# Optimization experiments

Hardware: AMD Instinct MI355X
Metric: run time of the kernel (lower is better)

## Reference

```python
import jax, jax.numpy as jnp
import numpy as np

B, S, D, H = 4, 2048, 1024, 16
DH = D // H  # 64

def setup_inputs() -> dict:
    key = jax.random.key(0)
    k0, k1, k2, k3 = jax.random.split(key, 4)
    x = jax.random.normal(k0, (B, S, D), dtype=jnp.float32)
    # Linear layers use random_normal init, shape (D, D), no bias.
    Wq = jax.random.normal(k1, (D, D), dtype=jnp.float32) * 0.05
    Wk = jax.random.normal(k2, (D, D), dtype=jnp.float32) * 0.05
    Wv = jax.random.normal(k3, (D, D), dtype=jnp.float32) * 0.05
    return {"encoder_input": x, "Wq": Wq, "Wk": Wk, "Wv": Wv}

def reference(encoder_input, Wq, Wk, Wv):
    x = encoder_input
    n_heads = H
    # Per-document projections, batched: [B,S,D]
    q = jnp.einsum('bsd,de->bse', x, Wq)
    k = jnp.einsum('bsd,de->bse', x, Wk)
    v = jnp.einsum('bsd,de->bse', x, Wv)
    # np.split(..., H, axis=-1) == reshape last dim to [H, DH]
    q = q.reshape(B, S, n_heads, DH)
    k = k.reshape(B, S, n_heads, DH)
    v = v.reshape(B, S, n_heads, DH)
    # Scaled dot-product attention; NOTE: original divides by N_HEADS, not sqrt(d_head)
    scores = jnp.einsum('bqhd,bkhd->bhqk', q, k) / jnp.float32(n_heads)
    attn = jax.nn.softmax(scores, axis=-1)
    out = jnp.einsum('bhqk,bkhd->bqhd', attn, v)
    # Concatenate heads along last dim -> [B,S,D]
    return out.reshape(B, S, D)
```

## Files before the change

### kernel.cpp

```cpp
#include <hip/hip_runtime.h>

typedef unsigned short u16;
typedef unsigned int   u32;
typedef __bf16 bf16x8 __attribute__((ext_vector_type(8)));
typedef __bf16 bf16x4 __attribute__((ext_vector_type(4)));
typedef float  f32x4  __attribute__((ext_vector_type(4)));
typedef u32    u32x4  __attribute__((ext_vector_type(4)));
typedef u32    u32x2  __attribute__((ext_vector_type(2)));
typedef u16    u16x8  __attribute__((ext_vector_type(8)));

#define MFMA16(a,b,c) __builtin_amdgcn_mfma_f32_16x16x32_bf16(a,b,c,0,0,0)

#define BB 4
#define SS 2048
#define DD 1024
#define HH 16
#define DH 64
#define MM 8192

#define QSCALE 0.0901684400555602f

#define WAIT_VM0() __builtin_amdgcn_s_waitcnt(0x0F70)

__device__ __forceinline__ u16 f2bf(float f) {
  u32 u = __builtin_bit_cast(u32, f);
  u += 0x7fffu + ((u >> 16) & 1u);
  return (u16)(u >> 16);
}

__device__ __forceinline__ void async16(const void* g, void* l) {
  __builtin_amdgcn_global_load_lds(
      (const __attribute__((address_space(1))) unsigned int*)g,
      (__attribute__((address_space(3))) unsigned int*)l, 16, 0, 0);
}

__global__ __launch_bounds__(256) void convert_x(
    const float* __restrict__ in, u16* __restrict__ out)
{
  const size_t stride = (size_t)gridDim.x * 256 * 8;
  for (size_t i = ((size_t)blockIdx.x * 256 + threadIdx.x) * 8;
       i < (size_t)MM * DD; i += stride) {
    f32x4 a = *(const f32x4*)(in + i);
    f32x4 b = *(const f32x4*)(in + i + 4);
    u32x2 ua = __builtin_bit_cast(u32x2, __builtin_convertvector(a, bf16x4));
    u32x2 ub = __builtin_bit_cast(u32x2, __builtin_convertvector(b, bf16x4));
    u32x4 v = {ua[0], ua[1], ub[0], ub[1]};
    *(u32x4*)(out + i) = v;
  }
}

__global__ __launch_bounds__(256) void fill_sig(float* __restrict__ out, int n)
{
  for (int i = blockIdx.x * 256 + threadIdx.x; i < n; i += gridDim.x * 256)
    out[i] = 3.0f;
}

__global__ __launch_bounds__(256) void convert_w(
    const float* __restrict__ w0, const float* __restrict__ w1,
    const float* __restrict__ w2, u16* __restrict__ WtAll)
{
  const int z = blockIdx.z;
  const float* W = (z == 0) ? w0 : ((z == 1) ? w1 : w2);
  u16* Wt = WtAll + (size_t)z * DD * DD;
  const int n0 = blockIdx.x * 64;
  const int k0 = blockIdx.y * 64;
  __shared__ u16 tile[64][65];
#pragma unroll
  for (int i = 0; i < 16; ++i) {
    int e = threadIdx.x + i * 256;
    int r = e >> 6, c = e & 63;
    tile[r][c] = f2bf(W[(size_t)(k0 + r) * DD + n0 + c]);
  }
  __syncthreads();
#pragma unroll
  for (int i = 0; i < 16; ++i) {
    int e = threadIdx.x + i * 256;
    int r = e >> 6, c = e & 63;
    Wt[(size_t)(n0 + r) * DD + k0 + c] = tile[c][r];
  }
}

__global__ __launch_bounds__(256) void qkv_gemm(
    const u16* __restrict__ X, const u16* __restrict__ WtAll,
    u16* __restrict__ QKV)
{
  const int z = blockIdx.z;
  const u16* Wt = WtAll + (size_t)z * DD * DD;
  u16* Y = QKV + (size_t)z * MM * DD;
  const int m0 = blockIdx.x * 128;
  const int n0 = blockIdx.y * 128;
  const int t = threadIdx.x;
  const int ln = t & 63;
  const int w  = t >> 6;
  const int cl = ln & 15;
  const int qd = ln >> 4;
  const int wm = (w & 1) * 64;
  const int wn = (w >> 1) * 64;
  const int srow   = ln >> 2;
  const int schunk = (ln & 3) * 8;

  __shared__ __align__(16) u16 Asm[128 * 32];
  __shared__ __align__(16) u16 Bsm[128 * 32];

  const f32x4 fzero = {0.f, 0.f, 0.f, 0.f};
  f32x4 acc[4][4];
#pragma unroll
  for (int i = 0; i < 4; ++i)
#pragma unroll
    for (int j = 0; j < 4; ++j) acc[i][j] = fzero;

  for (int k0 = 0; k0 < DD; k0 += 32) {
    __syncthreads();
#pragma unroll
    for (int c = 0; c < 2; ++c) {
      async16(X  + (size_t)(m0 + c * 64 + w * 16 + srow) * DD + k0 + schunk,
              Asm + (c * 64 + w * 16) * 32);
      async16(Wt + (size_t)(n0 + c * 64 + w * 16 + srow) * DD + k0 + schunk,
              Bsm + (c * 64 + w * 16) * 32);
    }
    WAIT_VM0();
    __syncthreads();

    bf16x8 af[4], bf[4];
#pragma unroll
    for (int mb = 0; mb < 4; ++mb)
      af[mb] = *(const bf16x8*)&Asm[(wm + mb * 16 + cl) * 32 + qd * 8];
#pragma unroll
    for (int nb = 0; nb < 4; ++nb)
      bf[nb] = *(const bf16x8*)&Bsm[(wn + nb * 16 + cl) * 32 + qd * 8];
#pragma unroll
    for (int mb = 0; mb < 4; ++mb)
#pragma unroll
      for (int nb = 0; nb < 4; ++nb)
        acc[mb][nb] = MFMA16(af[mb], bf[nb], acc[mb][nb]);
  }

  const float scl = (z == 0) ? QSCALE : 1.0f;
#pragma unroll
  for (int mb = 0; mb < 4; ++mb) {
#pragma unroll
    for (int r = 0; r < 4; ++r) {
      const size_t row = (size_t)(m0 + wm + mb * 16 + qd * 4 + r) * DD;
      f32x4 v = {acc[mb][0][r] * scl, acc[mb][1][r] * scl,
                 acc[mb][2][r] * scl, acc[mb][3][r] * scl};
      bf16x4 bv = __builtin_convertvector(v, bf16x4);
#pragma unroll
      for (int nb = 0; nb < 4; ++nb)
        *(__bf16*)&Y[row + n0 + wn + nb * 16 + cl] = bv[nb];
    }
  }
}

__global__ __launch_bounds__(256) void vtrans(
    const u16* __restrict__ V, u16* __restrict__ VtG)
{
  const int b = blockIdx.z;
  const int h = blockIdx.y;
  const int s0 = blockIdx.x * 64;
  __shared__ u16 tile[64][65];
#pragma unroll
  for (int i = 0; i < 16; ++i) {
    int e = threadIdx.x + i * 256;
    int r = e >> 6, c = e & 63;
    tile[r][c] = V[(size_t)(b * SS + s0 + r) * DD + h * DH + c];
  }
  __syncthreads();
#pragma unroll
  for (int i = 0; i < 16; ++i) {
    int e = threadIdx.x + i * 256;
    int r = e >> 6, c = e & 63;
    VtG[((size_t)(b * HH + h) * DH + r) * SS + s0 + c] = tile[c][r];
  }
}

__global__ __launch_bounds__(256, 2) void attn_kernel(
    const u16* __restrict__ QKV, const u16* __restrict__ VtG,
    float* __restrict__ Out)
{
  const int bh = blockIdx.x;
  const int b = bh >> 4;
  const int h = bh & 15;
  const int q0 = blockIdx.y * 128;
  const int t = threadIdx.x;
  const int ln = t & 63;
  const int w  = t >> 6;
  const int cl = ln & 15;
  const int qd = ln >> 4;
  const int srow   = ln >> 2;
  const int schunk = (ln & 3) * 8;

  const u16* Qg = QKV;
  const u16* Kg = QKV + (size_t)MM * DD;

  __shared__ __align__(16) u16 smem[20992];
  u16* const Pl = smem + 16384;

  const size_t qoffA = (size_t)(b * SS + q0 + w * 16 + cl) * DD + h * DH;
  const size_t qoffB = qoffA + (size_t)64 * DD;
  const bf16x8 qfA0 = *(const bf16x8*)(Qg + qoffA + qd * 8);
  const bf16x8 qfA1 = *(const bf16x8*)(Qg + qoffA + 32 + qd * 8);
  const bf16x8 qfB0 = *(const bf16x8*)(Qg + qoffB + qd * 8);
  const bf16x8 qfB1 = *(const bf16x8*)(Qg + qoffB + 32 + qd * 8);

  const f32x4 fzero = {0.f, 0.f, 0.f, 0.f};
  f32x4 oaccA[4], oaccB[4];
#pragma unroll
  for (int mt = 0; mt < 4; ++mt) { oaccA[mt] = fzero; oaccB[mt] = fzero; }
  float lsumA = 0.f, lsumB = 0.f;

  const size_t kgbase  = (size_t)b * SS * DD + (size_t)h * DH;
  const size_t vtgbase = ((size_t)(b * HH + h)) * DH * SS;

  u16* const Pw  = Pl + (w * 16 + cl) * 72;
  const u16* const Pr = Pl + (w * 16 + cl) * 72;

  auto stage = [&](int kt, int bi) {
    u16* kb = smem + bi * 4096;
    u16* vb = smem + 8192 + bi * 4096;
#pragma unroll
    for (int s = 0; s < 2; ++s) {
      async16(Kg  + kgbase + (size_t)(kt + w * 16 + srow) * DD + s * 32 + schunk,
              kb + (s * 64 + w * 16) * 32);
      async16(VtG + vtgbase + (size_t)(w * 16 + srow) * SS + kt + s * 32 + schunk,
              vb + (s * 64 + w * 16) * 32);
    }
  };

  stage(0, 0);

  for (int it = 0; it < SS / 64; ++it) {
    const int cur = it & 1;
    WAIT_VM0();
    __syncthreads();
    if (it + 1 < SS / 64) stage((it + 1) * 64, cur ^ 1);

    const u16* Kh = smem + cur * 4096;
    const u16* Vh = smem + 8192 + cur * 4096;

    f32x4 stA[4], stB[4];
#pragma unroll
    for (int mt = 0; mt < 4; ++mt) {
      bf16x8 kf0 = *(const bf16x8*)&Kh[(mt * 16 + cl) * 32 + qd * 8];
      bf16x8 kf1 = *(const bf16x8*)&Kh[(64 + mt * 16 + cl) * 32 + qd * 8];
      f32x4 za = fzero, zb = fzero;
      za = MFMA16(kf0, qfA0, za); za = MFMA16(kf1, qfA1, za);
      zb = MFMA16(kf0, qfB0, zb); zb = MFMA16(kf1, qfB1, zb);
      stA[mt] = za; stB[mt] = zb;
    }

    bf16x8 vf0[4], vf1[4];
#pragma unroll
    for (int mt = 0; mt < 4; ++mt) {
      vf0[mt] = *(const bf16x8*)&Vh[(mt * 16 + cl) * 32 + qd * 8];
      vf1[mt] = *(const bf16x8*)&Vh[(64 + mt * 16 + cl) * 32 + qd * 8];
    }

#pragma unroll
    for (int mt = 0; mt < 4; ++mt) {
      f32x4 p;
#pragma unroll
      for (int r = 0; r < 4; ++r) {
        p[r] = __builtin_amdgcn_exp2f(stA[mt][r]);
        lsumA += p[r];
      }
      *(u32x2*)(Pw + mt * 16 + qd * 4) =
          __builtin_bit_cast(u32x2, __builtin_convertvector(p, bf16x4));
    }

    f32x4 pB[4];
#pragma unroll
    for (int mt = 0; mt < 4; ++mt) {
#pragma unroll
      for (int r = 0; r < 4; ++r) {
        pB[mt][r] = __builtin_amdgcn_exp2f(stB[mt][r]);
        lsumB += pB[mt][r];
      }
    }

    {
      const bf16x8 pf0 = *(const bf16x8*)(Pr + qd * 8);
      const bf16x8 pf1 = *(const bf16x8*)(Pr + 32 + qd * 8);
#pragma unroll
      for (int mt = 0; mt < 4; ++mt) {
        oaccA[mt] = MFMA16(vf0[mt], pf0, oaccA[mt]);
        oaccA[mt] = MFMA16(vf1[mt], pf1, oaccA[mt]);
      }
    }

#pragma unroll
    for (int mt = 0; mt < 4; ++mt)
      *(u32x2*)(Pw + mt * 16 + qd * 4) =
          __builtin_bit_cast(u32x2, __builtin_convertvector(pB[mt], bf16x4));
    {
      const bf16x8 pf0 = *(const bf16x8*)(Pr + qd * 8);
      const bf16x8 pf1 = *(const bf16x8*)(Pr + 32 + qd * 8);
#pragma unroll
      for (int mt = 0; mt < 4; ++mt) {
        oaccB[mt] = MFMA16(vf0[mt], pf0, oaccB[mt]);
        oaccB[mt] = MFMA16(vf1[mt], pf1, oaccB[mt]);
      }
    }
  }

  lsumA += __shfl_xor(lsumA, 16);
  lsumA += __shfl_xor(lsumA, 32);
  lsumB += __shfl_xor(lsumB, 16);
  lsumB += __shfl_xor(lsumB, 32);

  __syncthreads();
  float* Ol = (float*)smem;
  const int q   = ln >> 2;
  const int seg = ln & 3;
  const float* src = Ol + w * 1088 + q * 68 + seg * 16;

  const float invA = 1.f / lsumA;
#pragma unroll
  for (int mt = 0; mt < 4; ++mt) {
    f32x4 vv = oaccA[mt];
#pragma unroll
    for (int r = 0; r < 4; ++r) vv[r] *= invA;
    *(f32x4*)(Ol + w * 1088 + cl * 68 + mt * 16 + qd * 4) = vv;
  }
  {
    float* dst = Out + (size_t)(b * SS + q0 + w * 16 + q) * DD + h * DH + seg * 16;
#pragma unroll
    for (int i = 0; i < 4; ++i)
      *(f32x4*)(dst + i * 4) = *(const f32x4*)(src + i * 4);
  }

  const float invB = 1.f / lsumB;
#pragma unroll
  for (int mt = 0; mt < 4; ++mt) {
    f32x4 vv = oaccB[mt];
#pragma unroll
    for (int r = 0; r < 4; ++r) vv[r] *= invB;
    *(f32x4*)(Ol + w * 1088 + cl * 68 + mt * 16 + qd * 4) = vv;
  }
  {
    float* dst = Out + (size_t)(b * SS + q0 + 64 + w * 16 + q) * DD + h * DH + seg * 16;
#pragma unroll
    for (int i = 0; i < 4; ++i)
      *(f32x4*)(dst + i * 4) = *(const f32x4*)(src + i * 4);
  }
}

extern "C" void kernel_launch(void* const* d_in, const int* in_sizes, int n_in,
                              void* d_out, int out_size, void* d_ws, size_t ws_size,
                              hipStream_t stream)
{
  const float* x  = (const float*)d_in[0];
  const float* wq = (const float*)d_in[1];
  const float* wk = (const float*)d_in[2];
  const float* wv = (const float*)d_in[3];
  float* out = (float*)d_out;

  const size_t need = ((size_t)MM * DD + 3 * (size_t)DD * DD +
                       3 * (size_t)MM * DD + (size_t)MM * DD) * sizeof(u16);
  if (ws_size < need) {
    fill_sig<<<1024, 256, 0, stream>>>(out, out_size);
    return;
  }

  u16* xs  = (u16*)d_ws;
  u16* wt  = xs + (size_t)MM * DD;
  u16* qkv = wt + (size_t)3 * DD * DD;
  u16* vtg = qkv + (size_t)3 * MM * DD;

  convert_x<<<2048, 256, 0, stream>>>(x, xs);
  convert_w<<<dim3(16, 16, 3), 256, 0, stream>>>(wq, wk, wv, wt);
  qkv_gemm<<<dim3(64, 8, 3), 256, 0, stream>>>(xs, wt, qkv);
  vtrans<<<dim3(32, HH, BB), 256, 0, stream>>>(qkv + (size_t)2 * MM * DD, vtg);
  attn_kernel<<<dim3(HH * BB, SS / 128, 1), 256, 0, stream>>>(qkv, vtg, out);
}
```

Measured before the change: 243.7 us.

## Widen GEMM K-tile, double attention query tile, swizzle K/V shared memory

The QKV GEMM now stages 64-wide K slices per barrier instead of 32, which halves the number of sync/wait rounds. The attention kernel processes 256 queries per block instead of 128, so each staged K/V tile is reused across four query groups and global K/V traffic drops. K and V tiles are also XOR-swizzled in shared memory to reduce LDS bank conflicts. In exchange, register pressure goes up (four output accumulators), which may lower occupancy, and the grid has fewer blocks.

```diff
diff --git a/kernel.cpp b/kernel.cpp
--- a/kernel.cpp
+++ b/kernel.cpp
@@ -96,11 +96,11 @@
   const int qd = ln >> 4;
   const int wm = (w & 1) * 64;
   const int wn = (w >> 1) * 64;
-  const int srow   = ln >> 2;
-  const int schunk = (ln & 3) * 8;
-
-  __shared__ __align__(16) u16 Asm[128 * 32];
-  __shared__ __align__(16) u16 Bsm[128 * 32];
+  const int srow8   = ln >> 3;
+  const int schunk8 = (ln & 7) * 8;
+
+  __shared__ __align__(16) u16 Asm[128 * 64];
+  __shared__ __align__(16) u16 Bsm[128 * 64];
 
   const f32x4 fzero = {0.f, 0.f, 0.f, 0.f};
   f32x4 acc[4][4];
@@ -109,30 +109,33 @@
 #pragma unroll
     for (int j = 0; j < 4; ++j) acc[i][j] = fzero;
 
-  for (int k0 = 0; k0 < DD; k0 += 32) {
+  for (int k0 = 0; k0 < DD; k0 += 64) {
     __syncthreads();
 #pragma unroll
-    for (int c = 0; c < 2; ++c) {
-      async16(X  + (size_t)(m0 + c * 64 + w * 16 + srow) * DD + k0 + schunk,
-              Asm + (c * 64 + w * 16) * 32);
-      async16(Wt + (size_t)(n0 + c * 64 + w * 16 + srow) * DD + k0 + schunk,
-              Bsm + (c * 64 + w * 16) * 32);
+    for (int c = 0; c < 4; ++c) {
+      async16(X  + (size_t)(m0 + c * 32 + w * 8 + srow8) * DD + k0 + schunk8,
+              Asm + (c * 32 + w * 8) * 64);
+      async16(Wt + (size_t)(n0 + c * 32 + w * 8 + srow8) * DD + k0 + schunk8,
+              Bsm + (c * 32 + w * 8) * 64);
     }
     WAIT_VM0();
     __syncthreads();
 
-    bf16x8 af[4], bf[4];
-#pragma unroll
-    for (int mb = 0; mb < 4; ++mb)
-      af[mb] = *(const bf16x8*)&Asm[(wm + mb * 16 + cl) * 32 + qd * 8];
-#pragma unroll
-    for (int nb = 0; nb < 4; ++nb)
-      bf[nb] = *(const bf16x8*)&Bsm[(wn + nb * 16 + cl) * 32 + qd * 8];
-#pragma unroll
-    for (int mb = 0; mb < 4; ++mb)
+#pragma unroll
+    for (int kk = 0; kk < 2; ++kk) {
+      bf16x8 af[4], bf[4];
+#pragma unroll
+      for (int mb = 0; mb < 4; ++mb)
+        af[mb] = *(const bf16x8*)&Asm[(wm + mb * 16 + cl) * 64 + kk * 32 + qd * 8];
 #pragma unroll
       for (int nb = 0; nb < 4; ++nb)
-        acc[mb][nb] = MFMA16(af[mb], bf[nb], acc[mb][nb]);
+        bf[nb] = *(const bf16x8*)&Bsm[(wn + nb * 16 + cl) * 64 + kk * 32 + qd * 8];
+#pragma unroll
+      for (int mb = 0; mb < 4; ++mb)
+#pragma unroll
+        for (int nb = 0; nb < 4; ++nb)
+          acc[mb][nb] = MFMA16(af[mb], bf[nb], acc[mb][nb]);
+    }
   }
 
   const float scl = (z == 0) ? QSCALE : 1.0f;
@@ -180,14 +183,15 @@
   const int bh = blockIdx.x;
   const int b = bh >> 4;
   const int h = bh & 15;
-  const int q0 = blockIdx.y * 128;
+  const int q0 = blockIdx.y * 256;
   const int t = threadIdx.x;
   const int ln = t & 63;
   const int w  = t >> 6;
   const int cl = ln & 15;
   const int qd = ln >> 4;
-  const int srow   = ln >> 2;
-  const int schunk = (ln & 3) * 8;
+  const int srow = ln >> 2;
+  const int swz = (((ln & 3) ^ ((srow >> 1) & 3)) << 3);
+  const int sx = ((qd ^ ((cl >> 1) & 3)) << 3);
 
   const u16* Qg = QKV;
   const u16* Kg = QKV + (size_t)MM * DD;
@@ -195,18 +199,23 @@
   __shared__ __align__(16) u16 smem[20992];
   u16* const Pl = smem + 16384;
 
-  const size_t qoffA = (size_t)(b * SS + q0 + w * 16 + cl) * DD + h * DH;
-  const size_t qoffB = qoffA + (size_t)64 * DD;
-  const bf16x8 qfA0 = *(const bf16x8*)(Qg + qoffA + qd * 8);
-  const bf16x8 qfA1 = *(const bf16x8*)(Qg + qoffA + 32 + qd * 8);
-  const bf16x8 qfB0 = *(const bf16x8*)(Qg + qoffB + qd * 8);
-  const bf16x8 qfB1 = *(const bf16x8*)(Qg + qoffB + 32 + qd * 8);
+  const size_t qoff0 = (size_t)(b * SS + q0 + w * 16 + cl) * DD + h * DH;
+  const bf16x8 qf0a = *(const bf16x8*)(Qg + qoff0 + qd * 8);
+  const bf16x8 qf0b = *(const bf16x8*)(Qg + qoff0 + 32 + qd * 8);
+  const bf16x8 qf1a = *(const bf16x8*)(Qg + qoff0 + (size_t)64 * DD + qd * 8);
+  const bf16x8 qf1b = *(const bf16x8*)(Qg + qoff0 + (size_t)64 * DD + 32 + qd * 8);
+  const bf16x8 qf2a = *(const bf16x8*)(Qg + qoff0 + (size_t)128 * DD + qd * 8);
+  const bf16x8 qf2b = *(const bf16x8*)(Qg + qoff0 + (size_t)128 * DD + 32 + qd * 8);
+  const bf16x8 qf3a = *(const bf16x8*)(Qg + qoff0 + (size_t)192 * DD + qd * 8);
+  const bf16x8 qf3b = *(const bf16x8*)(Qg + qoff0 + (size_t)192 * DD + 32 + qd * 8);
 
   const f32x4 fzero = {0.f, 0.f, 0.f, 0.f};
-  f32x4 oaccA[4], oaccB[4];
-#pragma unroll
-  for (int mt = 0; mt < 4; ++mt) { oaccA[mt] = fzero; oaccB[mt] = fzero; }
-  float lsumA = 0.f, lsumB = 0.f;
+  f32x4 oacc0[4], oacc1[4], oacc2[4], oacc3[4];
+#pragma unroll
+  for (int mt = 0; mt < 4; ++mt) {
+    oacc0[mt] = fzero; oacc1[mt] = fzero; oacc2[mt] = fzero; oacc3[mt] = fzero;
+  }
+  float lsum0 = 0.f, lsum1 = 0.f, lsum2 = 0.f, lsum3 = 0.f;
 
   const size_t kgbase  = (size_t)b * SS * DD + (size_t)h * DH;
   const size_t vtgbase = ((size_t)(b * HH + h)) * DH * SS;
@@ -219,12 +228,67 @@
     u16* vb = smem + 8192 + bi * 4096;
 #pragma unroll
     for (int s = 0; s < 2; ++s) {
-      async16(Kg  + kgbase + (size_t)(kt + w * 16 + srow) * DD + s * 32 + schunk,
+      async16(Kg  + kgbase + (size_t)(kt + w * 16 + srow) * DD + s * 32 + swz,
               kb + (s * 64 + w * 16) * 32);
-      async16(VtG + vtgbase + (size_t)(w * 16 + srow) * SS + kt + s * 32 + schunk,
+      async16(VtG + vtgbase + (size_t)(w * 16 + srow) * SS + kt + s * 32 + swz,
               vb + (s * 64 + w * 16) * 32);
     }
   };
+
+#define PAIR(QA0, QA1, QB0, QB1, OA, OB, LA, LB) do {                         \
+    f32x4 stA[4], stB[4];                                                     \
+    _Pragma("unroll")                                                         \
+    for (int mt = 0; mt < 4; ++mt) {                                          \
+      bf16x8 kf0 = *(const bf16x8*)&Kh[(mt * 16 + cl) * 32 + sx];             \
+      bf16x8 kf1 = *(const bf16x8*)&Kh[(64 + mt * 16 + cl) * 32 + sx];        \
+      f32x4 za = fzero, zb = fzero;                                           \
+      za = MFMA16(kf0, QA0, za); za = MFMA16(kf1, QA1, za);                   \
+      zb = MFMA16(kf0, QB0, zb); zb = MFMA16(kf1, QB1, zb);                   \
+      stA[mt] = za; stB[mt] = zb;                                             \
+    }                                                                         \
+    _Pragma("unroll")                                                         \
+    for (int mt = 0; mt < 4; ++mt) {                                          \
+      f32x4 p;                                                                \
+      _Pragma("unroll")                                                       \
+      for (int r = 0; r < 4; ++r) {                                           \
+        p[r] = __builtin_amdgcn_exp2f(stA[mt][r]);                            \
+        LA += p[r];                                                           \
+      }                                                                       \
+      *(u32x2*)(Pw + mt * 16 + qd * 4) =                                      \
+          __builtin_bit_cast(u32x2, __builtin_convertvector(p, bf16x4));      \
+    }                                                                         \
+    f32x4 pB[4];                                                              \
+    _Pragma("unroll")                                                         \
+    for (int mt = 0; mt < 4; ++mt) {                                          \
+      _Pragma("unroll")                                                       \
+      for (int r = 0; r < 4; ++r) {                                           \
+        pB[mt][r] = __builtin_amdgcn_exp2f(stB[mt][r]);                       \
+        LB += pB[mt][r];                                                      \
+      }                                                                       \
+    }                                                                         \
+    {                                                                         \
+      const bf16x8 pf0 = *(const bf16x8*)(Pr + qd * 8);                       \
+      const bf16x8 pf1 = *(const bf16x8*)(Pr + 32 + qd * 8);                  \
+      _Pragma("unroll")                                                       \
+      for (int mt = 0; mt < 4; ++mt) {                                        \
+        OA[mt] = MFMA16(vf0[mt], pf0, OA[mt]);                                \
+        OA[mt] = MFMA16(vf1[mt], pf1, OA[mt]);                                \
+      }                                                                       \
+    }                                                                         \
+    _Pragma("unroll")                                                         \
+    for (int mt = 0; mt < 4; ++mt)                                            \
+      *(u32x2*)(Pw + mt * 16 + qd * 4) =                                      \
+          __builtin_bit_cast(u32x2, __builtin_convertvector(pB[mt], bf16x4)); \
+    {                                                                         \
+      const bf16x8 pf0 = *(const bf16x8*)(Pr + qd * 8);                       \
+      const bf16x8 pf1 = *(const bf16x8*)(Pr + 32 + qd * 8);                  \
+      _Pragma("unroll")                                                       \
+      for (int mt = 0; mt < 4; ++mt) {                                        \
+        OB[mt] = MFMA16(vf0[mt], pf0, OB[mt]);                                \
+        OB[mt] = MFMA16(vf1[mt], pf1, OB[mt]);                                \
+      }                                                                       \
+    }                                                                         \
+  } while (0)
 
   stage(0, 0);
 
@@ -237,75 +301,21 @@
     const u16* Kh = smem + cur * 4096;
     const u16* Vh = smem + 8192 + cur * 4096;
 
-    f32x4 stA[4], stB[4];
+    bf16x8 vf0[4], vf1[4];
 #pragma unroll
     for (int mt = 0; mt < 4; ++mt) {
-      bf16x8 kf0 = *(const bf16x8*)&Kh[(mt * 16 + cl) * 32 + qd * 8];
-      bf16x8 kf1 = *(const bf16x8*)&Kh[(64 + mt * 16 + cl) * 32 + qd * 8];
-      f32x4 za = fzero, zb = fzero;
-      za = MFMA16(kf0, qfA0, za); za = MFMA16(kf1, qfA1, za);
-      zb = MFMA16(kf0, qfB0, zb); zb = MFMA16(kf1, qfB1, zb);
-      stA[mt] = za; stB[mt] = zb;
-    }
-
-    bf16x8 vf0[4], vf1[4];
-#pragma unroll
-    for (int mt = 0; mt < 4; ++mt) {
-      vf0[mt] = *(const bf16x8*)&Vh[(mt * 16 + cl) * 32 + qd * 8];
-      vf1[mt] = *(const bf16x8*)&Vh[(64 + mt * 16 + cl) * 32 + qd * 8];
-    }
-
-#pragma unroll
-    for (int mt = 0; mt < 4; ++mt) {
-      f32x4 p;
-#pragma unroll
-      for (int r = 0; r < 4; ++r) {
-        p[r] = __builtin_amdgcn_exp2f(stA[mt][r]);
-        lsumA += p[r];
-      }
-      *(u32x2*)(Pw + mt * 16 + qd * 4) =
-          __builtin_bit_cast(u32x2, __builtin_convertvector(p, bf16x4));
-    }
-
-    f32x4 pB[4];
-#pragma unroll
-    for (int mt = 0; mt < 4; ++mt) {
-#pragma unroll
-      for (int r = 0; r < 4; ++r) {
-        pB[mt][r] = __builtin_amdgcn_exp2f(stB[mt][r]);
-        lsumB += pB[mt][r];
-      }
-    }
-
-    {
-      const bf16x8 pf0 = *(const bf16x8*)(Pr + qd * 8);
-      const bf16x8 pf1 = *(const bf16x8*)(Pr + 32 + qd * 8);
-#pragma unroll
-      for (int mt = 0; mt < 4; ++mt) {
-        oaccA[mt] = MFMA16(vf0[mt], pf0, oaccA[mt]);
-        oaccA[mt] = MFMA16(vf1[mt], pf1, oaccA[mt]);
-      }
-    }
-
-#pragma unroll
-    for (int mt = 0; mt < 4; ++mt)
-      *(u32x2*)(Pw + mt * 16 + qd * 4) =
-          __builtin_bit_cast(u32x2, __builtin_convertvector(pB[mt], bf16x4));
-    {
-      const bf16x8 pf0 = *(const bf16x8*)(Pr + qd * 8);
-      const bf16x8 pf1 = *(const bf16x8*)(Pr + 32 + qd * 8);
-#pragma unroll
-      for (int mt = 0; mt < 4; ++mt) {
-        oaccB[mt] = MFMA16(vf0[mt], pf0, oaccB[mt]);
-        oaccB[mt] = MFMA16(vf1[mt], pf1, oaccB[mt]);
-      }
-    }
-  }
-
-  lsumA += __shfl_xor(lsumA, 16);
-  lsumA += __shfl_xor(lsumA, 32);
-  lsumB += __shfl_xor(lsumB, 16);
-  lsumB += __shfl_xor(lsumB, 32);
+      vf0[mt] = *(const bf16x8*)&Vh[(mt * 16 + cl) * 32 + sx];
+      vf1[mt] = *(const bf16x8*)&Vh[(64 + mt * 16 + cl) * 32 + sx];
+    }
+
+    PAIR(qf0a, qf0b, qf1a, qf1b, oacc0, oacc1, lsum0, lsum1);
+    PAIR(qf2a, qf2b, qf3a, qf3b, oacc2, oacc3, lsum2, lsum3);
+  }
+
+  lsum0 += __shfl_xor(lsum0, 16); lsum0 += __shfl_xor(lsum0, 32);
+  lsum1 += __shfl_xor(lsum1, 16); lsum1 += __shfl_xor(lsum1, 32);
+  lsum2 += __shfl_xor(lsum2, 16); lsum2 += __shfl_xor(lsum2, 32);
+  lsum3 += __shfl_xor(lsum3, 16); lsum3 += __shfl_xor(lsum3, 32);
 
   __syncthreads();
   float* Ol = (float*)smem;
@@ -313,35 +323,31 @@
   const int seg = ln & 3;
   const float* src = Ol + w * 1088 + q * 68 + seg * 16;
 
-  const float invA = 1.f / lsumA;
-#pragma unroll
-  for (int mt = 0; mt < 4; ++mt) {
-    f32x4 vv = oaccA[mt];
-#pragma unroll
-    for (int r = 0; r < 4; ++r) vv[r] *= invA;
-    *(f32x4*)(Ol + w * 1088 + cl * 68 + mt * 16 + qd * 4) = vv;
-  }
-  {
-    float* dst = Out + (size_t)(b * SS + q0 + w * 16 + q) * DD + h * DH + seg * 16;
-#pragma unroll
-    for (int i = 0; i < 4; ++i)
-      *(f32x4*)(dst + i * 4) = *(const f32x4*)(src + i * 4);
-  }
-
-  const float invB = 1.f / lsumB;
-#pragma unroll
-  for (int mt = 0; mt < 4; ++mt) {
-    f32x4 vv = oaccB[mt];
-#pragma unroll
-    for (int r = 0; r < 4; ++r) vv[r] *= invB;
-    *(f32x4*)(Ol + w * 1088 + cl * 68 + mt * 16 + qd * 4) = vv;
-  }
-  {
-    float* dst = Out + (size_t)(b * SS + q0 + 64 + w * 16 + q) * DD + h * DH + seg * 16;
-#pragma unroll
-    for (int i = 0; i < 4; ++i)
-      *(f32x4*)(dst + i * 4) = *(const f32x4*)(src + i * 4);
-  }
+#define EPI(OA, LS, SOFF) do {                                                \
+    const float inv = 1.f / (LS);                                             \
+    _Pragma("unroll")                                                         \
+    for (int mt = 0; mt < 4; ++mt) {                                          \
+      f32x4 vv = OA[mt];                                                      \
+      _Pragma("unroll")                                                       \
+      for (int r = 0; r < 4; ++r) vv[r] *= inv;                               \
+      *(f32x4*)(Ol + w * 1088 + cl * 68 + mt * 16 + qd * 4) = vv;             \
+    }                                                                         \
+    {                                                                         \
+      float* dst = Out + (size_t)(b * SS + q0 + (SOFF) + w * 16 + q) * DD     \
+                       + h * DH + seg * 16;                                   \
+      _Pragma("unroll")                                                       \
+      for (int i = 0; i < 4; ++i)                                             \
+        *(f32x4*)(dst + i * 4) = *(const f32x4*)(src + i * 4);                \
+    }                                                                         \
+  } while (0)
+
+  EPI(oacc0, lsum0, 0);
+  EPI(oacc1, lsum1, 64);
+  EPI(oacc2, lsum2, 128);
+  EPI(oacc3, lsum3, 192);
+
+#undef EPI
+#undef PAIR
 }
 
 extern "C" void kernel_launch(void* const* d_in, const int* in_sizes, int n_in,
@@ -370,5 +376,5 @@
   convert_w<<<dim3(16, 16, 3), 256, 0, stream>>>(wq, wk, wv, wt);
   qkv_gemm<<<dim3(64, 8, 3), 256, 0, stream>>>(xs, wt, qkv);
   vtrans<<<dim3(32, HH, BB), 256, 0, stream>>>(qkv + (size_t)2 * MM * DD, vtg);
-  attn_kernel<<<dim3(HH * BB, SS / 128, 1), 256, 0, stream>>>(qkv, vtg, out);
-}
+  attn_kernel<<<dim3(HH * BB, SS / 256, 1), 256, 0, stream>>>(qkv, vtg, out);
+}
```

Result: slower. 253.2 us (+3.9%).
